# Kernel optimization log

Hardware: AMD Instinct MI355X
Metric: run time of the kernel (lower is better)

Reference implementation:

```python
import jax, jax.numpy as jnp
import numpy as np

B, T, E = 2, 2048, 1024
H, D = 8, 512
ROPE_BASE = 10000.0


def apply_rope(x):
    # x: [B, H, T, D] -- rotary positional embedding, half-split convention
    t = x.shape[2]
    d = x.shape[3]
    inv_freq = 1.0 / (ROPE_BASE ** (jnp.arange(0, d, 2, dtype=jnp.float32) / d))  # [D/2]
    ang = jnp.arange(t, dtype=jnp.float32)[:, None] * inv_freq[None, :]           # [T, D/2]
    cos = jnp.cos(ang)[None, None].astype(x.dtype)
    sin = jnp.sin(ang)[None, None].astype(x.dtype)
    x1, x2 = jnp.split(x, 2, axis=-1)
    return jnp.concatenate([x1 * cos - x2 * sin, x1 * sin + x2 * cos], axis=-1)


def setup_inputs() -> dict:
    key = jax.random.key(0)
    ks = jax.random.split(key, 5)
    s_in = 1.0 / np.sqrt(E)
    s_out = 1.0 / np.sqrt(H * D)
    return {
        "x": jax.random.normal(ks[0], (B, T, E), dtype=jnp.float32),
        "Wq": jax.random.normal(ks[1], (H * D, E), dtype=jnp.float32) * s_in,
        "Wk": jax.random.normal(ks[2], (H * D, E), dtype=jnp.float32) * s_in,
        "Wv": jax.random.normal(ks[3], (H * D, E), dtype=jnp.float32) * s_in,
        "Wo": jax.random.normal(ks[4], (E, H * D), dtype=jnp.float32) * s_out,
    }


def reference(x, Wq, Wk, Wv, Wo):
    b, t, e = x.shape
    # QKV projections (bias-free Linear: x @ W.T), reshape to [B, H, T, D]
    q = (x @ Wq.T).reshape(b, t, H, D).transpose(0, 2, 1, 3)
    k = (x @ Wk.T).reshape(b, t, H, D).transpose(0, 2, 1, 3)
    v = (x @ Wv.T).reshape(b, t, H, D).transpose(0, 2, 1, 3)
    # RoPE on q and k
    q = apply_rope(q)
    k = apply_rope(k)
    # scaled dot-product attention with causal mask
    scale = 1.0 / jnp.sqrt(jnp.asarray(D, dtype=x.dtype))
    scores = jnp.einsum("bhqd,bhkd->bhqk", q, k) * scale
    causal = jnp.tril(jnp.ones((t, t), dtype=bool))
    scores = jnp.where(causal[None, None], scores, jnp.asarray(-jnp.inf, dtype=scores.dtype))
    probs = jax.nn.softmax(scores, axis=-1)  # explicitly materialized, as in source
    attn = jnp.einsum("bhqk,bhkd->bhqd", probs, v)
    out = attn.transpose(0, 2, 1, 3).reshape(b, t, H * D) @ Wo.T
    return out
```

## Files before the change

### kernel.cpp

```cpp
#include <hip/hip_runtime.h>


#define DEV __device__ __forceinline__

using bf16x8  = __attribute__((ext_vector_type(8))) short;
using floatx4 = __attribute__((ext_vector_type(4))) float;

#define MFMA16(a, b, c) __builtin_amdgcn_mfma_f32_16x16x32_bf16((a), (b), (c), 0, 0, 0)

DEV unsigned short f2bf(float f) {
  union { float f; unsigned int u; } c; c.f = f;
  unsigned int u = c.u + 0x7FFFu + ((c.u >> 16) & 1u);
  return (unsigned short)(u >> 16);
}
DEV float bf2f(unsigned short h) {
  union { unsigned int u; float f; } c; c.u = ((unsigned int)h) << 16;
  return c.f;
}

DEV void ldsld16(const unsigned short* g, unsigned short* l) {
  __builtin_amdgcn_global_load_lds(
      (__attribute__((address_space(1))) void*)(g),
      (__attribute__((address_space(3))) void*)(l), 16, 0, 0);
}

__global__ void cast5_k(const float* __restrict__ x,  const float* __restrict__ wq,
                        const float* __restrict__ wk, const float* __restrict__ wv,
                        const float* __restrict__ wo,
                        unsigned short* __restrict__ xb,  unsigned short* __restrict__ wqb,
                        unsigned short* __restrict__ wkb, unsigned short* __restrict__ wvb,
                        unsigned short* __restrict__ wob) {
  const float* s; unsigned short* d;
  switch (blockIdx.y) {
    case 0: s = x;  d = xb;  break;
    case 1: s = wq; d = wqb; break;
    case 2: s = wk; d = wkb; break;
    case 3: s = wv; d = wvb; break;
    default: s = wo; d = wob; break;
  }
  int i = blockIdx.x * 256 + threadIdx.x;
  float4 v = ((const float4*)s)[i];
  uint2 o;
  o.x = (unsigned int)f2bf(v.x) | ((unsigned int)f2bf(v.y) << 16);
  o.y = (unsigned int)f2bf(v.z) | ((unsigned int)f2bf(v.w) << 16);
  ((uint2*)d)[i] = o;
}

__global__ __launch_bounds__(256) void qkv_gemm(
    const unsigned short* __restrict__ X,
    const unsigned short* __restrict__ Wq, const unsigned short* __restrict__ Wk,
    const unsigned short* __restrict__ Wv,
    unsigned short* __restrict__ Qo, unsigned short* __restrict__ Ko, unsigned short* __restrict__ Vo) {
  __shared__ __align__(16) unsigned short As[128 * 32];
  __shared__ __align__(16) unsigned short Bs[128 * 32];
  const int tid = threadIdx.x;
  const int wave = tid >> 6, lane = tid & 63, quad = lane >> 4, l16 = lane & 15;
  const int m0 = blockIdx.x * 128, n0 = blockIdx.y * 128;
  const int z = blockIdx.z;
  const unsigned short* W = (z == 0) ? Wq : (z == 1) ? Wk : Wv;
  const int wm = (wave >> 1) * 64, wn = (wave & 1) * 64;
  floatx4 acc[4][4];
#pragma unroll
  for (int i = 0; i < 4; ++i)
#pragma unroll
    for (int j = 0; j < 4; ++j) acc[i][j] = (floatx4){0.f, 0.f, 0.f, 0.f};

  const int r0 = wave * 32;
  const int lrow = lane >> 2, lchunk = (lane & 3) * 8;
  for (int k0 = 0; k0 < 1024; k0 += 32) {
    const unsigned short* ga = X + (size_t)(m0 + r0 + lrow) * 1024 + k0 + lchunk;
    const unsigned short* gb = W + (size_t)(n0 + r0 + lrow) * 1024 + k0 + lchunk;
    ldsld16(ga, As + r0 * 32);
    ldsld16(ga + (size_t)16 * 1024, As + r0 * 32 + 512);
    ldsld16(gb, Bs + r0 * 32);
    ldsld16(gb + (size_t)16 * 1024, Bs + r0 * 32 + 512);
    __syncthreads();
    bf16x8 af[4], bw[4];
#pragma unroll
    for (int i = 0; i < 4; ++i) af[i] = *(const bf16x8*)(As + (wm + i * 16 + l16) * 32 + quad * 8);
#pragma unroll
    for (int j = 0; j < 4; ++j) bw[j] = *(const bf16x8*)(Bs + (wn + j * 16 + l16) * 32 + quad * 8);
#pragma unroll
    for (int i = 0; i < 4; ++i)
#pragma unroll
      for (int j = 0; j < 4; ++j) acc[i][j] = MFMA16(af[i], bw[j], acc[i][j]);
    __syncthreads();
  }
#pragma unroll
  for (int i = 0; i < 4; ++i)
#pragma unroll
    for (int j = 0; j < 4; ++j) {
      int gn = n0 + wn + j * 16 + l16;
      int h = gn >> 9, d = gn & 511;
      int gm0 = m0 + wm + i * 16 + quad * 4;
      int b = gm0 >> 11, t0 = gm0 & 2047;
      if (z == 2) {
        unsigned short pk[4];
#pragma unroll
        for (int r = 0; r < 4; ++r) pk[r] = f2bf(acc[i][j][r]);
        size_t off = ((size_t)((b * 8 + h) * 64 + (t0 >> 5))) * 16384 + (size_t)d * 32 + (t0 & 31);
        *(uint2*)(Vo + off) = *(uint2*)pk;
      } else {
        unsigned short* P = (z == 0) ? Qo : Ko;
        size_t base = ((size_t)((b * 8 + h) * 2048 + t0)) * 512 + d;
#pragma unroll
        for (int r = 0; r < 4; ++r) P[base + (size_t)r * 512] = f2bf(acc[i][j][r]);
      }
    }
}

__global__ void rope_k(unsigned short* __restrict__ Q, unsigned short* __restrict__ K) {
  int idx = blockIdx.x * 256 + threadIdx.x;
  unsigned short* P = (idx & 8388608) ? K : Q;
  int r = idx & 8388607;
  int row = r >> 8;
  int i = r & 255;
  int t = row & 2047;
  size_t base = (size_t)row * 512;
  float x1 = bf2f(P[base + i]);
  float x2 = bf2f(P[base + i + 256]);
  float freq = expf(-(float)i * 0.03597789207803197f);
  float ang = (float)t * freq;
  float sv, cv;
  sincosf(ang, &sv, &cv);
  P[base + i]       = f2bf(x1 * cv - x2 * sv);
  P[base + i + 256] = f2bf(x1 * sv + x2 * cv);
}

__global__ __launch_bounds__(256, 3) void flash_attn(
    const unsigned short* __restrict__ Q, const unsigned short* __restrict__ K,
    const unsigned short* __restrict__ Vslab, unsigned short* __restrict__ attn,
    unsigned short* __restrict__ P1, float* __restrict__ ml1, float* __restrict__ ml2,
    int split) {
  __shared__ __align__(16) unsigned short Vs[512 * 32];
  __shared__ __align__(16) unsigned short Ps[2 * 512];
  __shared__ __align__(16) float Sred[2 * 2 * 512];
  const int tid = threadIdx.x;
  const int wave = tid >> 6, lane = tid & 63, quad = lane >> 4, l16 = lane & 15;
  const int pr = wave >> 1, hh = wave & 1;
  const int bh = blockIdx.x, b = bh >> 3, head = bh & 7;
  const int y = blockIdx.y;
  int qi, st0, stN, om;
  if (split) {
    if (y < 64) {
      qi = 63 - (y >> 1);
      int mid = (qi + 1) >> 1;
      if ((y & 1) == 0) { st0 = 0;   stN = mid;    om = 1; }
      else              { st0 = mid; stN = qi + 1; om = 2; }
    } else { qi = 95 - y; st0 = 0; stN = qi + 1; om = 0; }
  } else { qi = 63 - y; st0 = 0; stN = qi + 1; om = 0; }

  const size_t bhoff = (size_t)bh << 20;
  const unsigned short* Qp = Q + bhoff;
  const unsigned short* Kp = K + bhoff;
  const unsigned short* Vp = Vslab + bhoff;
  const int qb = qi * 32;

  bf16x8 qf[8];
  {
    const unsigned short* qrow = Qp + (size_t)(qb + pr * 16 + l16) * 512 + hh * 256 + quad * 8;
#pragma unroll
    for (int ks = 0; ks < 8; ++ks) qf[ks] = *(const bf16x8*)(qrow + ks * 32);
  }
  floatx4 o[16];
#pragma unroll
  for (int n = 0; n < 16; ++n) o[n] = (floatx4){0.f, 0.f, 0.f, 0.f};
  float m_[4], l_[4];
#pragma unroll
  for (int r = 0; r < 4; ++r) { m_[r] = -3.0e38f; l_[r] = 0.f; }

  {
    const unsigned short* g = Vp + (size_t)st0 * 16384 + (size_t)(wave * 8) * 512 + lane * 8;
    unsigned short* lp = Vs + wave * 8 * 512;
#pragma unroll
    for (int i = 0; i < 8; ++i) ldsld16(g + i * 512, lp + i * 512);
  }

  for (int st = st0; st < stN; ++st) {
    const int s0 = st * 32;
    floatx4 sc0 = (floatx4){0.f, 0.f, 0.f, 0.f}, sc1 = sc0;
    const unsigned short* kbase = Kp + hh * 256 + quad * 8;
#pragma unroll
    for (int half = 0; half < 2; ++half) {
      bf16x8 kb[8];
#pragma unroll
      for (int q4 = 0; q4 < 4; ++q4) {
        int ks = half * 4 + q4;
        kb[q4 * 2]     = *(const bf16x8*)(kbase + (size_t)(s0 + l16) * 512 + ks * 32);
        kb[q4 * 2 + 1] = *(const bf16x8*)(kbase + (size_t)(s0 + 16 + l16) * 512 + ks * 32);
      }
#pragma unroll
      for (int q4 = 0; q4 < 4; ++q4) {
        sc0 = MFMA16(qf[half * 4 + q4], kb[q4 * 2], sc0);
        sc1 = MFMA16(qf[half * 4 + q4], kb[q4 * 2 + 1], sc1);
      }
    }
    float* sw = Sred + (pr * 2 + hh) * 512;
    *(floatx4*)(sw + l16 * 16 + quad * 4) = sc0;
    *(floatx4*)(sw + (16 + l16) * 16 + quad * 4) = sc1;
    __syncthreads();
    {
      const float* srd = Sred + (pr * 2 + (1 - hh)) * 512;
      floatx4 r0 = *(const floatx4*)(srd + l16 * 16 + quad * 4);
      floatx4 r1 = *(const floatx4*)(srd + (16 + l16) * 16 + quad * 4);
#pragma unroll
      for (int r = 0; r < 4; ++r) { sc0[r] += r0[r]; sc1[r] += r1[r]; }
    }
    const float scale = 0.04419417382415922f;
    const int qrow0 = qb + pr * 16 + quad * 4;
    float pv0[4], pv1[4], mr[4];
#pragma unroll
    for (int r = 0; r < 4; ++r) {
      float a0 = sc0[r] * scale, a1 = sc1[r] * scale;
      if (s0 + l16 > qrow0 + r) a0 = -3.0e38f;
      if (s0 + 16 + l16 > qrow0 + r) a1 = -3.0e38f;
      pv0[r] = a0; pv1[r] = a1;
      mr[r] = fmaxf(a0, a1);
    }
#pragma unroll
    for (int off = 1; off < 16; off <<= 1)
#pragma unroll
      for (int r = 0; r < 4; ++r) mr[r] = fmaxf(mr[r], __shfl_xor(mr[r], off, 64));
    float alpha[4], rs[4];
#pragma unroll
    for (int r = 0; r < 4; ++r) {
      float mn = fmaxf(m_[r], mr[r]);
      alpha[r] = __expf(m_[r] - mn);
      m_[r] = mn;
      float p0 = __expf(pv0[r] - mn);
      float p1 = __expf(pv1[r] - mn);
      rs[r] = p0 + p1;
      Ps[pr * 512 + (quad * 4 + r) * 32 + hh * 16 + l16] = f2bf(hh ? p1 : p0);
    }
#pragma unroll
    for (int off = 1; off < 16; off <<= 1)
#pragma unroll
      for (int r = 0; r < 4; ++r) rs[r] += __shfl_xor(rs[r], off, 64);
#pragma unroll
    for (int r = 0; r < 4; ++r) l_[r] = l_[r] * alpha[r] + rs[r];
    __syncthreads();
    if (__any(alpha[0] + alpha[1] + alpha[2] + alpha[3] < 4.0f)) {
#pragma unroll
      for (int n = 0; n < 16; ++n)
#pragma unroll
        for (int r = 0; r < 4; ++r) o[n][r] *= alpha[r];
    }
    bf16x8 pf = *(const bf16x8*)(Ps + pr * 512 + l16 * 32 + quad * 8);
#pragma unroll
    for (int nt = 0; nt < 16; ++nt) {
      bf16x8 vf = *(const bf16x8*)(Vs + (size_t)(hh * 256 + nt * 16 + l16) * 32 + quad * 8);
      o[nt] = MFMA16(pf, vf, o[nt]);
    }
    __syncthreads();
    if (st + 1 < stN) {
      const unsigned short* g = Vp + (size_t)(st + 1) * 16384 + (size_t)(wave * 8) * 512 + lane * 8;
      unsigned short* lp = Vs + wave * 8 * 512;
#pragma unroll
      for (int i = 0; i < 8; ++i) ldsld16(g + i * 512, lp + i * 512);
    }
  }
  const int rbase = pr * 16 + quad * 4;
  int p1i = bh * 32 + (qi - 32);
  if (om == 1) {
    unsigned short* prow = P1 + ((size_t)p1i * 32 + rbase) * 512 + hh * 256 + l16;
#pragma unroll
    for (int nt = 0; nt < 16; ++nt)
#pragma unroll
      for (int r = 0; r < 4; ++r)
        prow[(size_t)r * 512 + nt * 16] = f2bf(o[nt][r]);
  } else {
    unsigned short* arow =
        attn + ((size_t)(b * 2048 + qb + rbase)) * 4096 + head * 512 + hh * 256 + l16;
    if (om == 0) {
      float inv[4];
#pragma unroll
      for (int r = 0; r < 4; ++r) inv[r] = 1.0f / l_[r];
#pragma unroll
      for (int nt = 0; nt < 16; ++nt)
#pragma unroll
        for (int r = 0; r < 4; ++r)
          arow[(size_t)r * 4096 + nt * 16] = f2bf(o[nt][r] * inv[r]);
    } else {
#pragma unroll
      for (int nt = 0; nt < 16; ++nt)
#pragma unroll
        for (int r = 0; r < 4; ++r)
          arow[(size_t)r * 4096 + nt * 16] = f2bf(o[nt][r]);
    }
  }
  if (om != 0 && hh == 0 && l16 == 0) {
    float* ml = (om == 1) ? ml1 : ml2;
#pragma unroll
    for (int r = 0; r < 4; ++r) {
      ml[(size_t)p1i * 64 + (rbase + r) * 2]     = m_[r];
      ml[(size_t)p1i * 64 + (rbase + r) * 2 + 1] = l_[r];
    }
  }
}

__global__ void combine_k(const unsigned short* __restrict__ P1,
                          const float* __restrict__ ml1, const float* __restrict__ ml2,
                          unsigned short* __restrict__ attn) {
  const int p = blockIdx.x;
  const int bh = p >> 5, qi = 32 + (p & 31), b = bh >> 3, head = bh & 7;
  const int tid = threadIdx.x;
#pragma unroll
  for (int it = 0; it < 8; ++it) {
    int idx = it * 256 + tid;
    int row = idx >> 6, c8 = (idx & 63) * 8;
    float m1 = ml1[(size_t)p * 64 + row * 2], l1 = ml1[(size_t)p * 64 + row * 2 + 1];
    float m2 = ml2[(size_t)p * 64 + row * 2], l2 = ml2[(size_t)p * 64 + row * 2 + 1];
    float M = fmaxf(m1, m2);
    float w1 = __expf(m1 - M), w2 = __expf(m2 - M);
    float inv = 1.0f / (l1 * w1 + l2 * w2);
    const unsigned short* o1 = P1 + ((size_t)p * 32 + row) * 512 + c8;
    unsigned short* ap = attn + ((size_t)(b * 2048 + qi * 32 + row)) * 4096 + head * 512 + c8;
    unsigned short res[8];
#pragma unroll
    for (int j = 0; j < 8; ++j)
      res[j] = f2bf((bf2f(o1[j]) * w1 + bf2f(ap[j]) * w2) * inv);
    *(bf16x8*)ap = *(bf16x8*)res;
  }
}

__global__ __launch_bounds__(256) void out_gemm(
    const unsigned short* __restrict__ A, const unsigned short* __restrict__ W,
    float* __restrict__ C) {
  __shared__ __align__(16) unsigned short As[128 * 32];
  __shared__ __align__(16) unsigned short Bs[128 * 32];
  const int tid = threadIdx.x;
  const int wave = tid >> 6, lane = tid & 63, quad = lane >> 4, l16 = lane & 15;
  const int m0 = blockIdx.x * 128, n0 = blockIdx.y * 128;
  const int kb = blockIdx.z * 1024;
  const int wm = (wave >> 1) * 64, wn = (wave & 1) * 64;
  floatx4 acc[4][4];
#pragma unroll
  for (int i = 0; i < 4; ++i)
#pragma unroll
    for (int j = 0; j < 4; ++j) acc[i][j] = (floatx4){0.f, 0.f, 0.f, 0.f};
  const int r0 = wave * 32;
  const int lrow = lane >> 2, lchunk = (lane & 3) * 8;
  for (int k0 = kb; k0 < kb + 1024; k0 += 32) {
    const unsigned short* ga = A + (size_t)(m0 + r0 + lrow) * 4096 + k0 + lchunk;
    const unsigned short* gb = W + (size_t)(n0 + r0 + lrow) * 4096 + k0 + lchunk;
    ldsld16(ga, As + r0 * 32);
    ldsld16(ga + (size_t)16 * 4096, As + r0 * 32 + 512);
    ldsld16(gb, Bs + r0 * 32);
    ldsld16(gb + (size_t)16 * 4096, Bs + r0 * 32 + 512);
    __syncthreads();
    bf16x8 af[4], bw[4];
#pragma unroll
    for (int i = 0; i < 4; ++i) af[i] = *(const bf16x8*)(As + (wm + i * 16 + l16) * 32 + quad * 8);
#pragma unroll
    for (int j = 0; j < 4; ++j) bw[j] = *(const bf16x8*)(Bs + (wn + j * 16 + l16) * 32 + quad * 8);
#pragma unroll
    for (int i = 0; i < 4; ++i)
#pragma unroll
      for (int j = 0; j < 4; ++j) acc[i][j] = MFMA16(af[i], bw[j], acc[i][j]);
    __syncthreads();
  }
#pragma unroll
  for (int i = 0; i < 4; ++i)
#pragma unroll
    for (int j = 0; j < 4; ++j) {
      int gn = n0 + wn + j * 16 + l16;
#pragma unroll
      for (int r = 0; r < 4; ++r) {
        int gm = m0 + wm + i * 16 + quad * 4 + r;
        unsafeAtomicAdd(&C[(size_t)gm * 1024 + gn], acc[i][j][r]);
      }
    }
}

extern "C" void kernel_launch(void* const* d_in, const int* in_sizes, int n_in,
                              void* d_out, int out_size, void* d_ws, size_t ws_size,
                              hipStream_t stream) {
  const float* x  = (const float*)d_in[0];
  const float* Wq = (const float*)d_in[1];
  const float* Wk = (const float*)d_in[2];
  const float* Wv = (const float*)d_in[3];
  const float* Wo = (const float*)d_in[4];
  float* out = (float*)d_out;
  char* ws = (char*)d_ws;
  const size_t MB = 1048576;
  unsigned short* xb    = (unsigned short*)(ws + 0 * MB);
  unsigned short* wqb   = (unsigned short*)(ws + 8 * MB);
  unsigned short* wkb   = (unsigned short*)(ws + 16 * MB);
  unsigned short* wvb   = (unsigned short*)(ws + 24 * MB);
  unsigned short* wob   = (unsigned short*)(ws + 32 * MB);
  unsigned short* Qb    = (unsigned short*)(ws + 40 * MB);
  unsigned short* Kb    = (unsigned short*)(ws + 72 * MB);
  unsigned short* Vb    = (unsigned short*)(ws + 104 * MB);
  unsigned short* attnb = (unsigned short*)(ws + 0 * MB);
  unsigned short* P1    = (unsigned short*)(ws + 136 * MB);
  float* ml1            = (float*)(ws + 152 * MB);
  float* ml2            = (float*)(ws + 152 * MB + 131072);
  const int split = (ws_size >= (size_t)160 * MB) ? 1 : 0;

  hipMemsetAsync(d_out, 0, (size_t)4096 * 1024 * 4, stream);

  cast5_k<<<dim3(4096, 5), 256, 0, stream>>>(x, Wq, Wk, Wv, Wo, xb, wqb, wkb, wvb, wob);
  qkv_gemm<<<dim3(32, 32, 3), 256, 0, stream>>>(xb, wqb, wkb, wvb, Qb, Kb, Vb);
  rope_k<<<65536, 256, 0, stream>>>(Qb, Kb);
  flash_attn<<<dim3(16, split ? 96 : 64), 256, 0, stream>>>(Qb, Kb, Vb, attnb, P1, ml1, ml2, split);
  if (split) combine_k<<<512, 256, 0, stream>>>(P1, ml1, ml2, attnb);
  out_gemm<<<dim3(32, 8, 4), 256, 0, stream>>>(attnb, wob, out);
}
```

Measured before the change: 704.4 us.

## Restructure flash attention to per-wave full-D rows with 64-key tiles, no LDS V

Flash attention now uses 2 waves per block, and each wave owns 16 query rows across the full head dim of 512. This removes the cross-wave split-D score reduction through shared memory and the block-wide barriers. Key tiles grow from 32 to 64 keys, the causal mask is only evaluated on diagonal tiles, and V fragments are read straight from global memory instead of being staged in LDS. The cost is much higher register pressure (32 accumulator tiles plus 16 Q fragments per wave), lower occupancy, and uncoalesced global V reads that lean on the cache. The ml buffers also move to make room for the larger P1 usage.

```diff
diff --git a/kernel.cpp b/kernel.cpp
--- a/kernel.cpp
+++ b/kernel.cpp
@@ -127,95 +127,80 @@
   P[base + i + 256] = f2bf(x1 * sv + x2 * cv);
 }
 
-__global__ __launch_bounds__(256, 3) void flash_attn(
+__global__ __launch_bounds__(128, 2) void flash_attn(
     const unsigned short* __restrict__ Q, const unsigned short* __restrict__ K,
     const unsigned short* __restrict__ Vslab, unsigned short* __restrict__ attn,
     unsigned short* __restrict__ P1, float* __restrict__ ml1, float* __restrict__ ml2,
     int split) {
-  __shared__ __align__(16) unsigned short Vs[512 * 32];
-  __shared__ __align__(16) unsigned short Ps[2 * 512];
-  __shared__ __align__(16) float Sred[2 * 2 * 512];
+  __shared__ __align__(16) unsigned short Ps[2 * 16 * 72];
   const int tid = threadIdx.x;
   const int wave = tid >> 6, lane = tid & 63, quad = lane >> 4, l16 = lane & 15;
-  const int pr = wave >> 1, hh = wave & 1;
   const int bh = blockIdx.x, b = bh >> 3, head = bh & 7;
   const int y = blockIdx.y;
   int qi, st0, stN, om;
   if (split) {
     if (y < 64) {
       qi = 63 - (y >> 1);
-      int mid = (qi + 1) >> 1;
-      if ((y & 1) == 0) { st0 = 0;   stN = mid;    om = 1; }
-      else              { st0 = mid; stN = qi + 1; om = 2; }
-    } else { qi = 95 - y; st0 = 0; stN = qi + 1; om = 0; }
-  } else { qi = 63 - y; st0 = 0; stN = qi + 1; om = 0; }
+      int tot = (qi >> 1) + 1, mid = tot >> 1;
+      if ((y & 1) == 0) { st0 = 0;   stN = mid; om = 1; }
+      else              { st0 = mid; stN = tot; om = 2; }
+    } else { qi = 95 - y; st0 = 0; stN = (qi >> 1) + 1; om = 0; }
+  } else { qi = 63 - y; st0 = 0; stN = (qi >> 1) + 1; om = 0; }
 
   const size_t bhoff = (size_t)bh << 20;
   const unsigned short* Qp = Q + bhoff;
   const unsigned short* Kp = K + bhoff;
   const unsigned short* Vp = Vslab + bhoff;
   const int qb = qi * 32;
-
-  bf16x8 qf[8];
+  const int qw0 = qb + wave * 16;
+
+  bf16x8 qf[16];
   {
-    const unsigned short* qrow = Qp + (size_t)(qb + pr * 16 + l16) * 512 + hh * 256 + quad * 8;
-#pragma unroll
-    for (int ks = 0; ks < 8; ++ks) qf[ks] = *(const bf16x8*)(qrow + ks * 32);
-  }
-  floatx4 o[16];
-#pragma unroll
-  for (int n = 0; n < 16; ++n) o[n] = (floatx4){0.f, 0.f, 0.f, 0.f};
+    const unsigned short* qrow = Qp + (size_t)(qw0 + l16) * 512 + quad * 8;
+#pragma unroll
+    for (int ks = 0; ks < 16; ++ks) qf[ks] = *(const bf16x8*)(qrow + ks * 32);
+  }
+  floatx4 o[32];
+#pragma unroll
+  for (int n = 0; n < 32; ++n) o[n] = (floatx4){0.f, 0.f, 0.f, 0.f};
   float m_[4], l_[4];
 #pragma unroll
   for (int r = 0; r < 4; ++r) { m_[r] = -3.0e38f; l_[r] = 0.f; }
 
-  {
-    const unsigned short* g = Vp + (size_t)st0 * 16384 + (size_t)(wave * 8) * 512 + lane * 8;
-    unsigned short* lp = Vs + wave * 8 * 512;
-#pragma unroll
-    for (int i = 0; i < 8; ++i) ldsld16(g + i * 512, lp + i * 512);
-  }
+  unsigned short* psw = Ps + wave * 1152;
 
   for (int st = st0; st < stN; ++st) {
-    const int s0 = st * 32;
-    floatx4 sc0 = (floatx4){0.f, 0.f, 0.f, 0.f}, sc1 = sc0;
-    const unsigned short* kbase = Kp + hh * 256 + quad * 8;
-#pragma unroll
-    for (int half = 0; half < 2; ++half) {
-      bf16x8 kb[8];
-#pragma unroll
-      for (int q4 = 0; q4 < 4; ++q4) {
-        int ks = half * 4 + q4;
-        kb[q4 * 2]     = *(const bf16x8*)(kbase + (size_t)(s0 + l16) * 512 + ks * 32);
-        kb[q4 * 2 + 1] = *(const bf16x8*)(kbase + (size_t)(s0 + 16 + l16) * 512 + ks * 32);
-      }
-#pragma unroll
-      for (int q4 = 0; q4 < 4; ++q4) {
-        sc0 = MFMA16(qf[half * 4 + q4], kb[q4 * 2], sc0);
-        sc1 = MFMA16(qf[half * 4 + q4], kb[q4 * 2 + 1], sc1);
-      }
-    }
-    float* sw = Sred + (pr * 2 + hh) * 512;
-    *(floatx4*)(sw + l16 * 16 + quad * 4) = sc0;
-    *(floatx4*)(sw + (16 + l16) * 16 + quad * 4) = sc1;
-    __syncthreads();
-    {
-      const float* srd = Sred + (pr * 2 + (1 - hh)) * 512;
-      floatx4 r0 = *(const floatx4*)(srd + l16 * 16 + quad * 4);
-      floatx4 r1 = *(const floatx4*)(srd + (16 + l16) * 16 + quad * 4);
-#pragma unroll
-      for (int r = 0; r < 4; ++r) { sc0[r] += r0[r]; sc1[r] += r1[r]; }
+    const int s0 = st * 64;
+    floatx4 sc[4];
+#pragma unroll
+    for (int c = 0; c < 4; ++c) sc[c] = (floatx4){0.f, 0.f, 0.f, 0.f};
+    const unsigned short* kr0 = Kp + (size_t)(s0 + l16) * 512 + quad * 8;
+#pragma unroll 4
+    for (int ks = 0; ks < 16; ++ks) {
+      bf16x8 k0 = *(const bf16x8*)(kr0 + ks * 32);
+      bf16x8 k1 = *(const bf16x8*)(kr0 + 16 * 512 + ks * 32);
+      bf16x8 k2 = *(const bf16x8*)(kr0 + 32 * 512 + ks * 32);
+      bf16x8 k3 = *(const bf16x8*)(kr0 + 48 * 512 + ks * 32);
+      sc[0] = MFMA16(qf[ks], k0, sc[0]);
+      sc[1] = MFMA16(qf[ks], k1, sc[1]);
+      sc[2] = MFMA16(qf[ks], k2, sc[2]);
+      sc[3] = MFMA16(qf[ks], k3, sc[3]);
     }
     const float scale = 0.04419417382415922f;
-    const int qrow0 = qb + pr * 16 + quad * 4;
-    float pv0[4], pv1[4], mr[4];
-#pragma unroll
-    for (int r = 0; r < 4; ++r) {
-      float a0 = sc0[r] * scale, a1 = sc1[r] * scale;
-      if (s0 + l16 > qrow0 + r) a0 = -3.0e38f;
-      if (s0 + 16 + l16 > qrow0 + r) a1 = -3.0e38f;
-      pv0[r] = a0; pv1[r] = a1;
-      mr[r] = fmaxf(a0, a1);
+    const bool need_mask = (s0 + 63 > qw0);
+    float mr[4];
+#pragma unroll
+    for (int r = 0; r < 4; ++r) mr[r] = -3.0e38f;
+#pragma unroll
+    for (int c = 0; c < 4; ++c) {
+      int scol = s0 + c * 16 + l16;
+#pragma unroll
+      for (int r = 0; r < 4; ++r) {
+        float a = sc[c][r] * scale;
+        if (need_mask && scol > qw0 + quad * 4 + r) a = -3.0e38f;
+        sc[c][r] = a;
+        mr[r] = fmaxf(mr[r], a);
+      }
     }
 #pragma unroll
     for (int off = 1; off < 16; off <<= 1)
@@ -227,68 +212,71 @@
       float mn = fmaxf(m_[r], mr[r]);
       alpha[r] = __expf(m_[r] - mn);
       m_[r] = mn;
-      float p0 = __expf(pv0[r] - mn);
-      float p1 = __expf(pv1[r] - mn);
-      rs[r] = p0 + p1;
-      Ps[pr * 512 + (quad * 4 + r) * 32 + hh * 16 + l16] = f2bf(hh ? p1 : p0);
-    }
+      rs[r] = 0.f;
+    }
+#pragma unroll
+    for (int c = 0; c < 4; ++c)
+#pragma unroll
+      for (int r = 0; r < 4; ++r) {
+        float p = __expf(sc[c][r] - m_[r]);
+        rs[r] += p;
+        psw[(quad * 4 + r) * 72 + c * 16 + l16] = f2bf(p);
+      }
 #pragma unroll
     for (int off = 1; off < 16; off <<= 1)
 #pragma unroll
       for (int r = 0; r < 4; ++r) rs[r] += __shfl_xor(rs[r], off, 64);
 #pragma unroll
     for (int r = 0; r < 4; ++r) l_[r] = l_[r] * alpha[r] + rs[r];
-    __syncthreads();
     if (__any(alpha[0] + alpha[1] + alpha[2] + alpha[3] < 4.0f)) {
 #pragma unroll
-      for (int n = 0; n < 16; ++n)
+      for (int n = 0; n < 32; ++n)
 #pragma unroll
         for (int r = 0; r < 4; ++r) o[n][r] *= alpha[r];
     }
-    bf16x8 pf = *(const bf16x8*)(Ps + pr * 512 + l16 * 32 + quad * 8);
-#pragma unroll
-    for (int nt = 0; nt < 16; ++nt) {
-      bf16x8 vf = *(const bf16x8*)(Vs + (size_t)(hh * 256 + nt * 16 + l16) * 32 + quad * 8);
-      o[nt] = MFMA16(pf, vf, o[nt]);
-    }
-    __syncthreads();
-    if (st + 1 < stN) {
-      const unsigned short* g = Vp + (size_t)(st + 1) * 16384 + (size_t)(wave * 8) * 512 + lane * 8;
-      unsigned short* lp = Vs + wave * 8 * 512;
-#pragma unroll
-      for (int i = 0; i < 8; ++i) ldsld16(g + i * 512, lp + i * 512);
-    }
-  }
-  const int rbase = pr * 16 + quad * 4;
-  int p1i = bh * 32 + (qi - 32);
+    bf16x8 pf0 = *(const bf16x8*)(psw + l16 * 72 + quad * 8);
+    bf16x8 pf1 = *(const bf16x8*)(psw + l16 * 72 + 32 + quad * 8);
+#pragma unroll
+    for (int c2 = 0; c2 < 2; ++c2) {
+      bf16x8 pf = c2 ? pf1 : pf0;
+      const unsigned short* vb = Vp + (size_t)(2 * st + c2) * 16384 + (size_t)l16 * 32 + quad * 8;
+#pragma unroll 8
+      for (int nt = 0; nt < 32; ++nt) {
+        bf16x8 vf = *(const bf16x8*)(vb + (size_t)nt * 512);
+        o[nt] = MFMA16(pf, vf, o[nt]);
+      }
+    }
+  }
+  const int rbase = wave * 16 + quad * 4;
+  const int p1i = bh * 32 + (qi - 32);
   if (om == 1) {
-    unsigned short* prow = P1 + ((size_t)p1i * 32 + rbase) * 512 + hh * 256 + l16;
-#pragma unroll
-    for (int nt = 0; nt < 16; ++nt)
+    unsigned short* prow = P1 + ((size_t)p1i * 32 + rbase) * 512 + l16;
+#pragma unroll
+    for (int nt = 0; nt < 32; ++nt)
 #pragma unroll
       for (int r = 0; r < 4; ++r)
         prow[(size_t)r * 512 + nt * 16] = f2bf(o[nt][r]);
   } else {
     unsigned short* arow =
-        attn + ((size_t)(b * 2048 + qb + rbase)) * 4096 + head * 512 + hh * 256 + l16;
+        attn + ((size_t)(b * 2048 + qb + rbase)) * 4096 + head * 512 + l16;
     if (om == 0) {
       float inv[4];
 #pragma unroll
       for (int r = 0; r < 4; ++r) inv[r] = 1.0f / l_[r];
 #pragma unroll
-      for (int nt = 0; nt < 16; ++nt)
+      for (int nt = 0; nt < 32; ++nt)
 #pragma unroll
         for (int r = 0; r < 4; ++r)
           arow[(size_t)r * 4096 + nt * 16] = f2bf(o[nt][r] * inv[r]);
     } else {
 #pragma unroll
-      for (int nt = 0; nt < 16; ++nt)
+      for (int nt = 0; nt < 32; ++nt)
 #pragma unroll
         for (int r = 0; r < 4; ++r)
           arow[(size_t)r * 4096 + nt * 16] = f2bf(o[nt][r]);
     }
   }
-  if (om != 0 && hh == 0 && l16 == 0) {
+  if (om != 0 && l16 == 0) {
     float* ml = (om == 1) ? ml1 : ml2;
 #pragma unroll
     for (int r = 0; r < 4; ++r) {
@@ -393,8 +381,8 @@
   unsigned short* Vb    = (unsigned short*)(ws + 104 * MB);
   unsigned short* attnb = (unsigned short*)(ws + 0 * MB);
   unsigned short* P1    = (unsigned short*)(ws + 136 * MB);
-  float* ml1            = (float*)(ws + 152 * MB);
-  float* ml2            = (float*)(ws + 152 * MB + 131072);
+  float* ml1            = (float*)(ws + 153 * MB);
+  float* ml2            = (float*)(ws + 153 * MB + 131072);
   const int split = (ws_size >= (size_t)160 * MB) ? 1 : 0;
 
   hipMemsetAsync(d_out, 0, (size_t)4096 * 1024 * 4, stream);
@@ -402,7 +390,7 @@
   cast5_k<<<dim3(4096, 5), 256, 0, stream>>>(x, Wq, Wk, Wv, Wo, xb, wqb, wkb, wvb, wob);
   qkv_gemm<<<dim3(32, 32, 3), 256, 0, stream>>>(xb, wqb, wkb, wvb, Qb, Kb, Vb);
   rope_k<<<65536, 256, 0, stream>>>(Qb, Kb);
-  flash_attn<<<dim3(16, split ? 96 : 64), 256, 0, stream>>>(Qb, Kb, Vb, attnb, P1, ml1, ml2, split);
+  flash_attn<<<dim3(16, split ? 96 : 64), 128, 0, stream>>>(Qb, Kb, Vb, attnb, P1, ml1, ml2, split);
   if (split) combine_k<<<512, 256, 0, stream>>>(P1, ml1, ml2, attnb);
   out_gemm<<<dim3(32, 8, 4), 256, 0, stream>>>(attnb, wob, out);
 }
```

New measurement: 1.878 ms. 2.67x slower.
